# Performance work log

Measured on AMD Instinct MI355X. Metric: run time of the kernel, lower is better.

The kernel has to match this reference:

```python
import jax, jax.numpy as jnp
import numpy as np

WINDOW = (2, 7, 7)
NUM_HEADS = 8


def _relative_position_index(ws):
    d, h, w = ws
    coords = np.stack(np.meshgrid(np.arange(d), np.arange(h), np.arange(w), indexing='ij'), 0)
    cf = coords.reshape(3, -1)                      # [3, N]
    rel = (cf[:, :, None] - cf[:, None, :]).transpose(1, 2, 0)  # [N, N, 3]
    rel[..., 0] += d - 1
    rel[..., 1] += h - 1
    rel[..., 2] += w - 1
    idx = rel[..., 0] * ((2 * h - 1) * (2 * w - 1)) + rel[..., 1] * (2 * w - 1) + rel[..., 2]
    return idx.astype(np.int32)                     # [N, N]

_REL_IDX = _relative_position_index(WINDOW)


def setup_inputs() -> dict:
    key = jax.random.key(0)
    ks = jax.random.split(key, 6)
    B_, N, C = 2048, 98, 256
    nW = 64
    table_size = (2 * WINDOW[0] - 1) * (2 * WINDOW[1] - 1) * (2 * WINDOW[2] - 1)  # 507
    return {
        'x': jax.random.normal(ks[0], (B_, N, C), jnp.float32),
        'mask': jax.random.normal(ks[1], (nW, N, N), jnp.float32),
        'qkv_w': jax.random.normal(ks[2], (C, 3 * C), jnp.float32) * 0.02,
        'proj_w': jax.random.normal(ks[3], (C, C), jnp.float32) * 0.02,
        'proj_b': jax.random.normal(ks[4], (C,), jnp.float32) * 0.02,
        'bias_table': jax.random.normal(ks[5], (table_size, NUM_HEADS), jnp.float32) * 0.02,
    }


def reference(x, mask, qkv_w, proj_w, proj_b, bias_table):
    B_, N, C = x.shape
    H = NUM_HEADS
    Dh = C // H
    scale = Dh ** (-0.5)

    qkv = jnp.einsum('bnc,cd->bnd', x, qkv_w)               # [B_, N, 3C]
    qkv = qkv.reshape(B_, N, 3, H, Dh).transpose(2, 0, 3, 1, 4)  # [3, B_, H, N, Dh]
    q, k, v = qkv[0], qkv[1], qkv[2]

    attn = jnp.einsum('bhnd,bhmd->bhnm', q * scale, k)      # [B_, H, N, N]

    rel_idx = jnp.asarray(_REL_IDX[:N, :N])
    bias = bias_table[rel_idx.reshape(-1)].reshape(N, N, H).transpose(2, 0, 1)  # [H, N, N]
    attn = attn + bias[None]

    nW = mask.shape[0]
    attn = attn.reshape(B_ // nW, nW, H, N, N) + mask[None, :, None, :, :]
    attn = attn.reshape(B_, H, N, N)
    attn = jax.nn.softmax(attn, axis=-1)

    out = jnp.einsum('bhnm,bhmd->bhnd', attn, v)            # [B_, H, N, Dh]
    out = out.transpose(0, 2, 1, 3).reshape(B_, N, C)
    out = jnp.einsum('bnc,cd->bnd', out, proj_w) + proj_b
    return out
```

## Files before the change

kernel.cpp:

```cpp
#include <hip/hip_runtime.h>
#include <stdint.h>

typedef __bf16 bf16_t;
typedef __bf16 bf16x8 __attribute__((ext_vector_type(8)));
typedef float f32x4 __attribute__((ext_vector_type(4)));

#define MFMA16(a, b, c) __builtin_amdgcn_mfma_f32_16x16x32_bf16(a, b, c, 0, 0, 0)

__device__ __forceinline__ void gload_lds16(const bf16_t* g, bf16_t* l) {
  __builtin_amdgcn_global_load_lds(
      (const __attribute__((address_space(1))) void*)g,
      (__attribute__((address_space(3))) void*)l, 16, 0, 0);
}

__device__ __forceinline__ int sw4(int i) {
  return ((i & 3) << 2) | ((i >> 2) & 3);
}

__global__ __launch_bounds__(256) void cvt_w2_k(const float* __restrict__ w1,
                                                bf16_t* __restrict__ o1,
                                                const float* __restrict__ w2,
                                                bf16_t* __restrict__ o2) {
  int blk = blockIdx.x, k = threadIdx.x;
  if (blk < 768) {
    o1[(size_t)blk * 256 + k] = (bf16_t)w1[(size_t)k * 768 + blk];
  } else {
    int n = blk - 768;
    o2[(size_t)n * 256 + k] = (bf16_t)w2[(size_t)k * 256 + n];
  }
}

template <bool AF32>
__global__ __launch_bounds__(256) void gemm256_t(const void* __restrict__ Av,
                                                 const bf16_t* __restrict__ BT,
                                                 int ncols,
                                                 bf16_t* __restrict__ outb,
                                                 float* __restrict__ outf,
                                                 const float* __restrict__ bias) {
  __shared__ __align__(16) bf16_t sA[128 * 64];
  __shared__ __align__(16) bf16_t sB[128 * 64];
  const int tid = threadIdx.x;
  const int lane = tid & 63, wave = tid >> 6;
  const int lm = lane & 15, quad = lane >> 4;

  int nwg = gridDim.x * gridDim.y;
  int L = blockIdx.y * gridDim.x + blockIdx.x;
  if ((nwg & 7) == 0) {
    int cpx = nwg >> 3;
    L = (L & 7) * cpx + (L >> 3);
  }
  const int bx = L % gridDim.x, by = L / gridDim.x;

  const int mBase = by * 128;
  const int nBase = bx * 128;
  const int wm = (wave >> 1) * 64, wn = (wave & 1) * 64;

  f32x4 acc[4][4];
#pragma unroll
  for (int i = 0; i < 4; i++)
#pragma unroll
    for (int j = 0; j < 4; j++) acc[i][j] = {0.f, 0.f, 0.f, 0.f};

  const bf16_t* Ab = AF32 ? nullptr : (const bf16_t*)Av + (size_t)mBase * 256;
  const float* Af = AF32 ? (const float*)Av + (size_t)mBase * 256 : nullptr;
  const bf16_t* Bb = BT + (size_t)nBase * 256;

  for (int kb = 0; kb < 4; ++kb) {
    const int k0 = kb * 64;
    if constexpr (AF32) {
      f32x4 fa[4][2];
#pragma unroll
      for (int it = 0; it < 4; ++it) {
        int cid = it * 256 + wave * 64 + lane;
        int row = cid >> 3, kcp = cid & 7;
        int kcl = kcp ^ (row & 7);
        const f32x4* src = (const f32x4*)(Af + (size_t)row * 256 + k0 + kcl * 8);
        fa[it][0] = src[0];
        fa[it][1] = src[1];
      }
#pragma unroll
      for (int it = 0; it < 4; ++it) {
        int cid = it * 256 + wave * 64 + lane;
        int row = cid >> 3, kcp = cid & 7;
        bf16_t* dstB = sB + (it * 256 + wave * 64) * 8;
        gload_lds16(Bb + (size_t)row * 256 + k0 + (kcp ^ (row & 7)) * 8, dstB);
        bf16x8 o = {(bf16_t)fa[it][0][0], (bf16_t)fa[it][0][1],
                    (bf16_t)fa[it][0][2], (bf16_t)fa[it][0][3],
                    (bf16_t)fa[it][1][0], (bf16_t)fa[it][1][1],
                    (bf16_t)fa[it][1][2], (bf16_t)fa[it][1][3]};
        *(bf16x8*)(sA + (size_t)cid * 8) = o;
      }
    } else {
#pragma unroll
      for (int it = 0; it < 4; ++it) {
        int cid = it * 256 + wave * 64 + lane;
        int row = cid >> 3, kcp = cid & 7;
        int kcl = kcp ^ (row & 7);
        bf16_t* dstA = sA + (it * 256 + wave * 64) * 8;
        bf16_t* dstB = sB + (it * 256 + wave * 64) * 8;
        gload_lds16(Ab + (size_t)row * 256 + k0 + kcl * 8, dstA);
        gload_lds16(Bb + (size_t)row * 256 + k0 + kcl * 8, dstB);
      }
    }
    __syncthreads();
#pragma unroll
    for (int kk = 0; kk < 64; kk += 32) {
      int c = (kk >> 3) + quad;
      bf16x8 af[4], bfr[4];
#pragma unroll
      for (int mt = 0; mt < 4; mt++) {
        int m = wm + mt * 16 + lm;
        af[mt] = *(const bf16x8*)(sA + m * 64 + ((c ^ (m & 7)) << 3));
      }
#pragma unroll
      for (int nt = 0; nt < 4; nt++) {
        int n = wn + nt * 16 + lm;
        bfr[nt] = *(const bf16x8*)(sB + n * 64 + ((c ^ (n & 7)) << 3));
      }
#pragma unroll
      for (int mt = 0; mt < 4; mt++)
#pragma unroll
        for (int nt = 0; nt < 4; nt++)
          acc[mt][nt] = MFMA16(af[mt], bfr[nt], acc[mt][nt]);
    }
    __syncthreads();
  }

  if (outb) {
#pragma unroll
    for (int mt = 0; mt < 4; mt++)
#pragma unroll
      for (int nt = 0; nt < 4; nt++) {
        int col = nBase + wn + nt * 16 + lm;
        int rbase = mBase + wm + mt * 16 + quad * 4;
#pragma unroll
        for (int r = 0; r < 4; r++)
          outb[(size_t)(rbase + r) * ncols + col] = (bf16_t)acc[mt][nt][r];
      }
  } else {
#pragma unroll
    for (int mt = 0; mt < 4; mt++)
#pragma unroll
      for (int nt = 0; nt < 4; nt++) {
        int col = nBase + wn + nt * 16 + lm;
        float bv = bias[col];
        int rbase = mBase + wm + mt * 16 + quad * 4;
#pragma unroll
        for (int r = 0; r < 4; r++)
          outf[(size_t)(rbase + r) * ncols + col] = acc[mt][nt][r] + bv;
      }
  }
}

__global__ __launch_bounds__(256, 4) void attn_win(
    const bf16_t* __restrict__ qkv, const float* __restrict__ mask,
    const float* __restrict__ btab, bf16_t* __restrict__ y) {
  __shared__ __align__(16) bf16_t sP[112 * 128];
  __shared__ __align__(16) bf16_t sVT[32 * 128];
  __shared__ float sTab[512];
  __shared__ int sU[112];

  const int tid = threadIdx.x;
  const int L = blockIdx.x;
  const int qd = L >> 4, rr = L & 15;
  const int g = rr >> 3, x = rr & 7;
  const int bidx = qd * 8 + x;
  const int b = bidx >> 2;
  const int h = ((bidx & 3) << 1) | g;
  const int lane = tid & 63, wave = tid >> 6;
  const int lm = lane & 15, quad = lane >> 4;

  {
    uint4 z = {0, 0, 0, 0};
    uint4* p = (uint4*)sP;
    for (int i = tid; i < 112 * 128 / 8; i += 256) p[i] = z;
  }
  for (int idx = tid; idx < 1024; idx += 256) {
    int d = idx >> 5, j = 96 + (idx & 31);
    if (j >= 98)
      sVT[d * 128 + (((j >> 3) ^ sw4(d & 15)) << 3) + (j & 7)] = (bf16_t)0.f;
  }
  for (int i = tid; i < 507; i += 256) sTab[i] = btab[i * 8 + h];
  if (tid < 112) {
    int n = tid;
    int d = n / 49, r = n - d * 49;
    int hh = r / 7, w = r - hh * 7;
    sU[tid] = (n < 98) ? (d * 169 + hh * 13 + w) : 0;
  }

  const bf16_t* qb = qkv + (size_t)b * 98 * 768 + h * 32;

  {
    int j = tid & 127, hf = tid >> 7;
    if (j < 98) {
#pragma unroll
      for (int t = 0; t < 2; t++) {
        int dc = hf + 2 * t;
        bf16x8 v8 = *(const bf16x8*)(qb + (size_t)j * 768 + 512 + dc * 8);
#pragma unroll
        for (int e = 0; e < 8; e++) {
          int d = dc * 8 + e;
          sVT[d * 128 + (((j >> 3) ^ sw4(d & 15)) << 3) + (j & 7)] = v8[e];
        }
      }
    }
  }
  __syncthreads();

  bf16x8 kf[7];
#pragma unroll
  for (int ct = 0; ct < 7; ct++)
    kf[ct] =
        *(const bf16x8*)(qb + (size_t)(ct * 16 + lm) * 768 + 256 + quad * 8);

  f32x4 s4[2][7];
#pragma unroll
  for (int rti = 0; rti < 2; rti++) {
    int rt = wave + rti * 4;
    if (rt <= 6) {
      bf16x8 qf = *(const bf16x8*)(qb + (size_t)(rt * 16 + lm) * 768 + quad * 8);
#pragma unroll
      for (int ct = 0; ct < 7; ct++) {
        f32x4 z = {0.f, 0.f, 0.f, 0.f};
        s4[rti][ct] = MFMA16(qf, kf[ct], z);
      }
    }
  }

  const float* mp = mask + (size_t)(b & 63) * 9604;
  const float scale = 0.17677669529663687f;
  float inv[2][4];

#pragma unroll
  for (int rti = 0; rti < 2; rti++) {
    int rt = wave + rti * 4;
    if (rt > 6) continue;
    int ib = rt * 16 + quad * 4;
    int ui[4], rb[4];
#pragma unroll
    for (int r = 0; r < 4; r++) {
      int i = ib + r;
      ui[r] = sU[i] + 253;
      rb[r] = (i < 98 ? i : 97) * 98;
    }
#pragma unroll
    for (int ct = 0; ct < 7; ct++) {
      int j = ct * 16 + lm;
      int uj = sU[j];
      int jc = j < 98 ? j : 97;
      bool jv = j < 98;
#pragma unroll
      for (int r = 0; r < 4; r++) {
        float v = s4[rti][ct][r] * scale + sTab[ui[r] - uj] + mp[rb[r] + jc];
        s4[rti][ct][r] = jv ? v : -1e30f;
      }
    }
#pragma unroll
    for (int r = 0; r < 4; r++) {
      float mx = s4[rti][0][r];
#pragma unroll
      for (int ct = 1; ct < 7; ct++) mx = fmaxf(mx, s4[rti][ct][r]);
#pragma unroll
      for (int o = 1; o < 16; o <<= 1) mx = fmaxf(mx, __shfl_xor(mx, o));
      float sum = 0.f;
#pragma unroll
      for (int ct = 0; ct < 7; ct++) {
        float e = __expf(s4[rti][ct][r] - mx);
        s4[rti][ct][r] = e;
        sum += e;
      }
#pragma unroll
      for (int o = 1; o < 16; o <<= 1) sum += __shfl_xor(sum, o);
      inv[rti][r] = 1.f / sum;
    }
#pragma unroll
    for (int ct = 0; ct < 7; ct++) {
      int c2 = 2 * ct + (lm >> 3);
      int j7 = lm & 7;
#pragma unroll
      for (int r = 0; r < 4; r++) {
        int i = ib + r;
        sP[i * 128 + ((c2 ^ (4 * r + quad)) << 3) + j7] =
            (bf16_t)s4[rti][ct][r];
      }
    }
  }
  __syncthreads();

  bf16x8 vf[2][4];
#pragma unroll
  for (int dt = 0; dt < 2; dt++)
#pragma unroll
    for (int kk = 0; kk < 4; kk++) {
      int d = dt * 16 + lm;
      vf[dt][kk] =
          *(const bf16x8*)(sVT + d * 128 + (((4 * kk + quad) ^ sw4(lm)) << 3));
    }
  bf16_t* yb = y + (size_t)b * 98 * 256 + h * 32;
#pragma unroll
  for (int rti = 0; rti < 2; rti++) {
    int rt = wave + rti * 4;
    if (rt > 6) continue;
    bf16x8 af[4];
#pragma unroll
    for (int kk = 0; kk < 4; kk++) {
      int i = rt * 16 + lm;
      af[kk] =
          *(const bf16x8*)(sP + i * 128 + (((4 * kk + quad) ^ sw4(lm)) << 3));
    }
#pragma unroll
    for (int dt = 0; dt < 2; dt++) {
      f32x4 o = {0.f, 0.f, 0.f, 0.f};
#pragma unroll
      for (int kk = 0; kk < 4; kk++) o = MFMA16(af[kk], vf[dt][kk], o);
#pragma unroll
      for (int r = 0; r < 4; r++) {
        int i = rt * 16 + quad * 4 + r;
        if (i < 98)
          yb[(size_t)i * 256 + dt * 16 + lm] = (bf16_t)(o[r] * inv[rti][r]);
      }
    }
  }
}

extern "C" void kernel_launch(void* const* d_in, const int* in_sizes, int n_in,
                              void* d_out, int out_size, void* d_ws,
                              size_t ws_size, hipStream_t stream) {
  const float* x = (const float*)d_in[0];
  const float* mask = (const float*)d_in[1];
  const float* qkv_w = (const float*)d_in[2];
  const float* proj_w = (const float*)d_in[3];
  const float* proj_b = (const float*)d_in[4];
  const float* btab = (const float*)d_in[5];
  float* out = (float*)d_out;

  char* ws = (char*)d_ws;
  bf16_t* qkv = (bf16_t*)ws;
  bf16_t* ybuf = (bf16_t*)(ws + 308281344);
  bf16_t* wT = (bf16_t*)(ws + 308281344 + 102760448);
  bf16_t* pT = (bf16_t*)(ws + 308281344 + 102760448 + 393216);

  cvt_w2_k<<<1024, 256, 0, stream>>>(qkv_w, wT, proj_w, pT);

  gemm256_t<true><<<dim3(6, 1568), 256, 0, stream>>>(x, wT, 768, qkv, nullptr,
                                                     nullptr);

  attn_win<<<16384, 256, 0, stream>>>(qkv, mask, btab, ybuf);

  gemm256_t<false><<<dim3(2, 1568), 256, 0, stream>>>(ybuf, pT, 256, nullptr,
                                                      out, proj_b);
}
```

Before: 729.1 us.

## Precompute combined bias+mask table and loop attention over four windows per block

Adds a prep kernel that builds, per window and head, a padded 112x112 table of relative-position bias plus mask (with -1e30 on padded columns), stored temporarily in the output buffer. The attention kernel then reads this table with one fmaf instead of gathering the bias table and mask and building index tables in shared memory. Each block now handles four batch entries that share the same mask window, so setup work is amortised, and the grid shrinks fourfold. Zeroing of sP is reduced to the padding columns, and a ghost region past the qkv buffer is zeroed to cover out-of-range row reads. The cost is an extra kernel pass and fewer, longer blocks.

```diff
diff --git a/kernel.cpp b/kernel.cpp
--- a/kernel.cpp
+++ b/kernel.cpp
@@ -27,6 +27,40 @@
   } else {
     int n = blk - 768;
     o2[(size_t)n * 256 + k] = (bf16_t)w2[(size_t)k * 256 + n];
+  }
+}
+
+__global__ __launch_bounds__(256) void prep_cmb(const float* __restrict__ mask,
+                                                const float* __restrict__ btab,
+                                                float* __restrict__ cmb,
+                                                bf16_t* __restrict__ qkv_ghost) {
+  __shared__ int sU[112];
+  __shared__ float sT[512];
+  const int tid = threadIdx.x;
+  const int w = blockIdx.x >> 3, h = blockIdx.x & 7;
+  if (tid < 112) {
+    int n = tid;
+    int d = n / 49, r = n - d * 49;
+    int hh = r / 7, ww = r - hh * 7;
+    sU[tid] = (n < 98) ? (d * 169 + hh * 13 + ww) : 0;
+  }
+  for (int i = tid; i < 512; i += 256) sT[i] = (i < 507) ? btab[i * 8 + h] : 0.f;
+  __syncthreads();
+  const float* mp = mask + (size_t)w * 9604;
+  float* cb = cmb + (size_t)blockIdx.x * 12544;
+  for (int idx = tid; idx < 12544; idx += 256) {
+    int i = idx / 112, j = idx - i * 112;
+    float v;
+    if (j < 98)
+      v = sT[253 + sU[i] - sU[j]] + mp[(i < 98 ? i : 97) * 98 + j];
+    else
+      v = -1e30f;
+    cb[idx] = v;
+  }
+  if (blockIdx.x == 0) {
+    bf16x8 z = {};
+    for (int t = tid; t < 14 * 768 / 8; t += 256)
+      *(bf16x8*)(qkv_ghost + (size_t)t * 8) = z;
   }
 }
 
@@ -153,171 +187,155 @@
 }
 
 __global__ __launch_bounds__(256, 4) void attn_win(
-    const bf16_t* __restrict__ qkv, const float* __restrict__ mask,
-    const float* __restrict__ btab, bf16_t* __restrict__ y) {
+    const bf16_t* __restrict__ qkv, const float* __restrict__ cmb,
+    bf16_t* __restrict__ y) {
   __shared__ __align__(16) bf16_t sP[112 * 128];
   __shared__ __align__(16) bf16_t sVT[32 * 128];
-  __shared__ float sTab[512];
-  __shared__ int sU[112];
 
   const int tid = threadIdx.x;
   const int L = blockIdx.x;
   const int qd = L >> 4, rr = L & 15;
   const int g = rr >> 3, x = rr & 7;
   const int bidx = qd * 8 + x;
-  const int b = bidx >> 2;
+  const int b0 = bidx >> 2;
   const int h = ((bidx & 3) << 1) | g;
   const int lane = tid & 63, wave = tid >> 6;
   const int lm = lane & 15, quad = lane >> 4;
 
-  {
+  if (tid < 224) {
+    int i = tid >> 1, c2 = 14 + (tid & 1);
     uint4 z = {0, 0, 0, 0};
-    uint4* p = (uint4*)sP;
-    for (int i = tid; i < 112 * 128 / 8; i += 256) p[i] = z;
+    *(uint4*)(sP + i * 128 + ((c2 ^ sw4(i & 15)) << 3)) = z;
   }
   for (int idx = tid; idx < 1024; idx += 256) {
     int d = idx >> 5, j = 96 + (idx & 31);
     if (j >= 98)
       sVT[d * 128 + (((j >> 3) ^ sw4(d & 15)) << 3) + (j & 7)] = (bf16_t)0.f;
   }
-  for (int i = tid; i < 507; i += 256) sTab[i] = btab[i * 8 + h];
-  if (tid < 112) {
-    int n = tid;
-    int d = n / 49, r = n - d * 49;
-    int hh = r / 7, w = r - hh * 7;
-    sU[tid] = (n < 98) ? (d * 169 + hh * 13 + w) : 0;
-  }
-
-  const bf16_t* qb = qkv + (size_t)b * 98 * 768 + h * 32;
-
-  {
-    int j = tid & 127, hf = tid >> 7;
-    if (j < 98) {
-#pragma unroll
-      for (int t = 0; t < 2; t++) {
-        int dc = hf + 2 * t;
-        bf16x8 v8 = *(const bf16x8*)(qb + (size_t)j * 768 + 512 + dc * 8);
-#pragma unroll
-        for (int e = 0; e < 8; e++) {
-          int d = dc * 8 + e;
-          sVT[d * 128 + (((j >> 3) ^ sw4(d & 15)) << 3) + (j & 7)] = v8[e];
-        }
-      }
-    }
-  }
-  __syncthreads();
-
-  bf16x8 kf[7];
-#pragma unroll
-  for (int ct = 0; ct < 7; ct++)
-    kf[ct] =
-        *(const bf16x8*)(qb + (size_t)(ct * 16 + lm) * 768 + 256 + quad * 8);
-
-  f32x4 s4[2][7];
-#pragma unroll
-  for (int rti = 0; rti < 2; rti++) {
-    int rt = wave + rti * 4;
-    if (rt <= 6) {
-      bf16x8 qf = *(const bf16x8*)(qb + (size_t)(rt * 16 + lm) * 768 + quad * 8);
+
+  const float* cb = cmb + (size_t)((b0 & 63) * 8 + h) * 12544;
+  const float scale = 0.17677669529663687f;
+
+  for (int it = 0; it < 4; ++it) {
+    const int b = b0 + it * 512;
+    const bf16_t* qb = qkv + (size_t)b * 75264 + h * 32;
+
+    if (it) __syncthreads();
+
+    {
+      int j = tid & 127, hf = tid >> 7;
+      if (j < 98) {
+#pragma unroll
+        for (int t = 0; t < 2; t++) {
+          int dc = hf + 2 * t;
+          bf16x8 v8 = *(const bf16x8*)(qb + (size_t)j * 768 + 512 + dc * 8);
+#pragma unroll
+          for (int e = 0; e < 8; e++) {
+            int d = dc * 8 + e;
+            sVT[d * 128 + (((j >> 3) ^ sw4(d & 15)) << 3) + (j & 7)] = v8[e];
+          }
+        }
+      }
+    }
+    __syncthreads();
+
+    bf16x8 kf[7];
+#pragma unroll
+    for (int ct = 0; ct < 7; ct++)
+      kf[ct] =
+          *(const bf16x8*)(qb + (size_t)(ct * 16 + lm) * 768 + 256 + quad * 8);
+
+    f32x4 s4[2][7];
+#pragma unroll
+    for (int rti = 0; rti < 2; rti++) {
+      int rt = wave + rti * 4;
+      if (rt <= 6) {
+        bf16x8 qf =
+            *(const bf16x8*)(qb + (size_t)(rt * 16 + lm) * 768 + quad * 8);
+#pragma unroll
+        for (int ct = 0; ct < 7; ct++) {
+          f32x4 z = {0.f, 0.f, 0.f, 0.f};
+          s4[rti][ct] = MFMA16(qf, kf[ct], z);
+        }
+      }
+    }
+
+    float inv[2][4];
+#pragma unroll
+    for (int rti = 0; rti < 2; rti++) {
+      int rt = wave + rti * 4;
+      if (rt > 6) continue;
+      int ib = rt * 16 + quad * 4;
 #pragma unroll
       for (int ct = 0; ct < 7; ct++) {
-        f32x4 z = {0.f, 0.f, 0.f, 0.f};
-        s4[rti][ct] = MFMA16(qf, kf[ct], z);
-      }
-    }
-  }
-
-  const float* mp = mask + (size_t)(b & 63) * 9604;
-  const float scale = 0.17677669529663687f;
-  float inv[2][4];
-
-#pragma unroll
-  for (int rti = 0; rti < 2; rti++) {
-    int rt = wave + rti * 4;
-    if (rt > 6) continue;
-    int ib = rt * 16 + quad * 4;
-    int ui[4], rb[4];
-#pragma unroll
-    for (int r = 0; r < 4; r++) {
-      int i = ib + r;
-      ui[r] = sU[i] + 253;
-      rb[r] = (i < 98 ? i : 97) * 98;
-    }
-#pragma unroll
-    for (int ct = 0; ct < 7; ct++) {
-      int j = ct * 16 + lm;
-      int uj = sU[j];
-      int jc = j < 98 ? j : 97;
-      bool jv = j < 98;
+        int j = ct * 16 + lm;
+#pragma unroll
+        for (int r = 0; r < 4; r++)
+          s4[rti][ct][r] = fmaf(s4[rti][ct][r], scale, cb[(ib + r) * 112 + j]);
+      }
 #pragma unroll
       for (int r = 0; r < 4; r++) {
-        float v = s4[rti][ct][r] * scale + sTab[ui[r] - uj] + mp[rb[r] + jc];
-        s4[rti][ct][r] = jv ? v : -1e30f;
-      }
-    }
-#pragma unroll
-    for (int r = 0; r < 4; r++) {
-      float mx = s4[rti][0][r];
-#pragma unroll
-      for (int ct = 1; ct < 7; ct++) mx = fmaxf(mx, s4[rti][ct][r]);
-#pragma unroll
-      for (int o = 1; o < 16; o <<= 1) mx = fmaxf(mx, __shfl_xor(mx, o));
-      float sum = 0.f;
+        float mx = s4[rti][0][r];
+#pragma unroll
+        for (int ct = 1; ct < 7; ct++) mx = fmaxf(mx, s4[rti][ct][r]);
+#pragma unroll
+        for (int o = 1; o < 16; o <<= 1) mx = fmaxf(mx, __shfl_xor(mx, o));
+        float sum = 0.f;
+#pragma unroll
+        for (int ct = 0; ct < 7; ct++) {
+          float e = __expf(s4[rti][ct][r] - mx);
+          s4[rti][ct][r] = e;
+          sum += e;
+        }
+#pragma unroll
+        for (int o = 1; o < 16; o <<= 1) sum += __shfl_xor(sum, o);
+        inv[rti][r] = 1.f / sum;
+      }
 #pragma unroll
       for (int ct = 0; ct < 7; ct++) {
-        float e = __expf(s4[rti][ct][r] - mx);
-        s4[rti][ct][r] = e;
-        sum += e;
-      }
-#pragma unroll
-      for (int o = 1; o < 16; o <<= 1) sum += __shfl_xor(sum, o);
-      inv[rti][r] = 1.f / sum;
-    }
-#pragma unroll
-    for (int ct = 0; ct < 7; ct++) {
-      int c2 = 2 * ct + (lm >> 3);
-      int j7 = lm & 7;
-#pragma unroll
-      for (int r = 0; r < 4; r++) {
-        int i = ib + r;
-        sP[i * 128 + ((c2 ^ (4 * r + quad)) << 3) + j7] =
-            (bf16_t)s4[rti][ct][r];
-      }
-    }
-  }
-  __syncthreads();
-
-  bf16x8 vf[2][4];
-#pragma unroll
-  for (int dt = 0; dt < 2; dt++)
-#pragma unroll
-    for (int kk = 0; kk < 4; kk++) {
-      int d = dt * 16 + lm;
-      vf[dt][kk] =
-          *(const bf16x8*)(sVT + d * 128 + (((4 * kk + quad) ^ sw4(lm)) << 3));
-    }
-  bf16_t* yb = y + (size_t)b * 98 * 256 + h * 32;
-#pragma unroll
-  for (int rti = 0; rti < 2; rti++) {
-    int rt = wave + rti * 4;
-    if (rt > 6) continue;
-    bf16x8 af[4];
-#pragma unroll
-    for (int kk = 0; kk < 4; kk++) {
-      int i = rt * 16 + lm;
-      af[kk] =
-          *(const bf16x8*)(sP + i * 128 + (((4 * kk + quad) ^ sw4(lm)) << 3));
-    }
-#pragma unroll
-    for (int dt = 0; dt < 2; dt++) {
-      f32x4 o = {0.f, 0.f, 0.f, 0.f};
-#pragma unroll
-      for (int kk = 0; kk < 4; kk++) o = MFMA16(af[kk], vf[dt][kk], o);
-#pragma unroll
-      for (int r = 0; r < 4; r++) {
-        int i = rt * 16 + quad * 4 + r;
-        if (i < 98)
-          yb[(size_t)i * 256 + dt * 16 + lm] = (bf16_t)(o[r] * inv[rti][r]);
+        int c2 = 2 * ct + (lm >> 3);
+        int j7 = lm & 7;
+#pragma unroll
+        for (int r = 0; r < 4; r++) {
+          int i = ib + r;
+          sP[i * 128 + ((c2 ^ (4 * r + quad)) << 3) + j7] =
+              (bf16_t)s4[rti][ct][r];
+        }
+      }
+    }
+
+    bf16x8 vf[2][4];
+#pragma unroll
+    for (int dt = 0; dt < 2; dt++)
+#pragma unroll
+      for (int kk = 0; kk < 4; kk++) {
+        int d = dt * 16 + lm;
+        vf[dt][kk] = *(const bf16x8*)(sVT + d * 128 +
+                                      (((4 * kk + quad) ^ sw4(lm)) << 3));
+      }
+    bf16_t* yb = y + (size_t)b * 98 * 256 + h * 32;
+#pragma unroll
+    for (int rti = 0; rti < 2; rti++) {
+      int rt = wave + rti * 4;
+      if (rt > 6) continue;
+      bf16x8 af[4];
+#pragma unroll
+      for (int kk = 0; kk < 4; kk++) {
+        int i = rt * 16 + lm;
+        af[kk] =
+            *(const bf16x8*)(sP + i * 128 + (((4 * kk + quad) ^ sw4(lm)) << 3));
+      }
+#pragma unroll
+      for (int dt = 0; dt < 2; dt++) {
+        f32x4 o = {0.f, 0.f, 0.f, 0.f};
+#pragma unroll
+        for (int kk = 0; kk < 4; kk++) o = MFMA16(af[kk], vf[dt][kk], o);
+#pragma unroll
+        for (int r = 0; r < 4; r++) {
+          int i = rt * 16 + quad * 4 + r;
+          if (i < 98)
+            yb[(size_t)i * 256 + dt * 16 + lm] = (bf16_t)(o[r] * inv[rti][r]);
+        }
       }
     }
   }
@@ -339,13 +357,16 @@
   bf16_t* ybuf = (bf16_t*)(ws + 308281344);
   bf16_t* wT = (bf16_t*)(ws + 308281344 + 102760448);
   bf16_t* pT = (bf16_t*)(ws + 308281344 + 102760448 + 393216);
-
+  float* cmb = out;
+  bf16_t* qkv_ghost = qkv + (size_t)200704 * 768;
+
+  prep_cmb<<<512, 256, 0, stream>>>(mask, btab, cmb, qkv_ghost);
   cvt_w2_k<<<1024, 256, 0, stream>>>(qkv_w, wT, proj_w, pT);
 
   gemm256_t<true><<<dim3(6, 1568), 256, 0, stream>>>(x, wT, 768, qkv, nullptr,
                                                      nullptr);
 
-  attn_win<<<16384, 256, 0, stream>>>(qkv, mask, btab, ybuf);
+  attn_win<<<4096, 256, 0, stream>>>(qkv, cmb, ybuf);
 
   gemm256_t<false><<<dim3(2, 1568), 256, 0, stream>>>(ybuf, pT, 256, nullptr,
                                                       out, proj_b);
```

After: 1.412 ms. 93.6% more time.
